# Kernel optimization log

Hardware: AMD Instinct MI355X
Metric: run time of the kernel (lower is better)

Reference implementation:

```python
import jax, jax.numpy as jnp
import numpy as np
import math

N_HEAD = 16
K_SPARSE = 64

def setup_inputs() -> dict:
    key = jax.random.key(0)
    ks = jax.random.split(key, 12)
    B, T, C = 1, 2048, 1024
    s = 0.02
    return {
        "x":   jax.random.normal(ks[0], (B, T, C), jnp.float32),
        "Wq":  jax.random.normal(ks[1], (C, C), jnp.float32) * s,
        "bq":  jax.random.normal(ks[2], (C,), jnp.float32) * s,
        "Wk":  jax.random.normal(ks[3], (C, C), jnp.float32) * s,
        "bk":  jax.random.normal(ks[4], (C,), jnp.float32) * s,
        "Wv":  jax.random.normal(ks[5], (C, C), jnp.float32) * s,
        "bv":  jax.random.normal(ks[6], (C,), jnp.float32) * s,
        "Wo":  jax.random.normal(ks[7], (C, C), jnp.float32) * s,
        "bo":  jax.random.normal(ks[8], (C,), jnp.float32) * s,
        "Wks": jax.random.normal(ks[9], (C,), jnp.float32) * s,
        "bks": jax.random.normal(ks[10], (), jnp.float32) * s,
    }

def reference(x, Wq, bq, Wk, bk, Wv, bv, Wo, bo, Wks, bks):
    B, T, C = x.shape
    nh = N_HEAD
    hs = C // nh
    k_val = min(K_SPARSE, T)

    # projections -> (B, nh, T, hs)   (torch Linear: x @ W.T + b)
    q = (x @ Wq.T + bq).reshape(B, T, nh, hs).transpose(0, 2, 1, 3)
    k = (x @ Wk.T + bk).reshape(B, T, nh, hs).transpose(0, 2, 1, 3)
    v = (x @ Wv.T + bv).reshape(B, T, nh, hs).transpose(0, 2, 1, 3)

    # key scorer: per-token scalar score (B, T)
    key_scores = x @ Wks + bks

    # causal masking of scores, then per-query top-k key selection
    pos = jnp.arange(T)
    causal = pos[None, :] <= pos[:, None]                      # (T, T), True where key<=query
    masked = jnp.where(causal[None], key_scores[:, None, :], -jnp.inf)  # (B, T, T)
    _, top_k_idx = jax.lax.top_k(masked, k_val)                # (B, T, k)
    top_k_idx = jnp.minimum(top_k_idx, pos[None, :, None])     # clamp to <= query pos

    # gather sparse keys/values: (B, nh, T, k, hs)
    bi = jnp.arange(B)[:, None, None, None]
    hi = jnp.arange(nh)[None, :, None, None]
    gi = top_k_idx[:, None, :, :]                              # (B, 1, T, k)
    sparse_k = k[bi, hi, gi]                                   # (B, nh, T, k, hs)
    sparse_v = v[bi, hi, gi]

    scale = 1.0 / math.sqrt(hs)
    logits = jnp.einsum('bhtd,bhtkd->bhtk', q, sparse_k) * scale
    probs = jax.nn.softmax(logits, axis=-1)
    out = jnp.einsum('bhtk,bhtkd->bhtd', probs, sparse_v)      # (B, nh, T, hs)
    out = out.transpose(0, 2, 1, 3).reshape(B, T, C)
    return out @ Wo.T + bo
```

## Files before the change

kernel.cpp:

```cpp
#include <hip/hip_runtime.h>
#include <hip/hip_bf16.h>
#include <cstdint>
#include <cstddef>

#define T_DIM 2048
#define C_DIM 1024
#define NH 16
#define HS 64
#define KSP 64

#define GBM 128
#define GBN 64
#define GBK 128
#define OBM 64
#define OBN 64

typedef short short8 __attribute__((ext_vector_type(8)));
typedef float f32x4 __attribute__((ext_vector_type(4)));
typedef _Float16 half2_t __attribute__((ext_vector_type(2)));

__device__ __forceinline__ float bfu2f(unsigned short u) {
  unsigned v = ((unsigned)u) << 16;
  return __builtin_bit_cast(float, v);
}
__device__ __forceinline__ unsigned short f2bfu(float f) {
  unsigned u = __builtin_bit_cast(unsigned, f);
  unsigned r = (u + 0x7fffu + ((u >> 16) & 1u)) >> 16;
  return (unsigned short)r;
}
__device__ __forceinline__ unsigned short f2h(float f) {
  _Float16 h = (_Float16)f;
  return __builtin_bit_cast(unsigned short, h);
}
__device__ __forceinline__ float bflo(unsigned u) {
  return __builtin_bit_cast(float, u << 16);
}
__device__ __forceinline__ float bfhi(unsigned u) {
  return __builtin_bit_cast(float, u & 0xffff0000u);
}

__device__ __forceinline__ float dot2h(unsigned kbits, unsigned qbits, float acc) {
#if __has_builtin(__builtin_amdgcn_fdot2)
  return __builtin_amdgcn_fdot2(__builtin_bit_cast(half2_t, kbits),
                                __builtin_bit_cast(half2_t, qbits), acc, false);
#else
  half2_t kk = __builtin_bit_cast(half2_t, kbits);
  half2_t qq = __builtin_bit_cast(half2_t, qbits);
  return acc + (float)kk.x * (float)qq.x + (float)kk.y * (float)qq.y;
#endif
}

#define GLOAD_LDS16(gp, lp)                                                  \
  __builtin_amdgcn_global_load_lds(                                          \
      (const __attribute__((address_space(1))) void*)(gp),                   \
      (__attribute__((address_space(3))) void*)(lp), 16, 0, 0)

#define NSCORE (T_DIM / 4)
#define NCONV ((T_DIM * C_DIM + 4 * C_DIM * C_DIM) / 4 / 256)
__global__ __launch_bounds__(256) void convert_scores_kernel(
    const float* __restrict__ x, const float* __restrict__ Wq,
    const float* __restrict__ Wk, const float* __restrict__ Wv,
    const float* __restrict__ Wo, const float* __restrict__ Wks,
    const float* __restrict__ bks,
    unsigned short* __restrict__ xb, unsigned short* __restrict__ Wqb,
    unsigned short* __restrict__ Wkb, unsigned short* __restrict__ Wvb,
    unsigned short* __restrict__ Wob, float* __restrict__ scores) {
  if (blockIdx.x < NSCORE) {
    const int t = blockIdx.x * 4 + (threadIdx.x >> 6);
    const int lane = threadIdx.x & 63;
    const float* xrow = x + (size_t)t * C_DIM;
    float acc = 0.f;
    #pragma unroll 4
    for (int i = lane; i < C_DIM; i += 64)
      acc += xrow[i] * Wks[i];
    #pragma unroll
    for (int o = 32; o; o >>= 1) acc += __shfl_xor(acc, o);
    if (lane == 0) scores[t] = acc + bks[0];
    return;
  }
  const int i = (blockIdx.x - NSCORE) * 256 + threadIdx.x;
  const int NX4 = T_DIM * C_DIM / 4;
  const int NW4 = C_DIM * C_DIM / 4;
  const float* src;
  unsigned short* dst;
  int j = i;
  if (j < NX4) { src = x; dst = xb; }
  else {
    j -= NX4;
    int w = j / NW4;
    j -= w * NW4;
    src = (w == 0) ? Wq : (w == 1) ? Wk : (w == 2) ? Wv : Wo;
    dst = (w == 0) ? Wqb : (w == 1) ? Wkb : (w == 2) ? Wvb : Wob;
  }
  float4 f = reinterpret_cast<const float4*>(src)[j];
  ushort4 o;
  o.x = f2bfu(f.x); o.y = f2bfu(f.y); o.z = f2bfu(f.z); o.w = f2bfu(f.w);
  reinterpret_cast<ushort4*>(dst)[j] = o;
}

__global__ __launch_bounds__(256) void rank_sort_kernel(
    const float* __restrict__ scores, int* __restrict__ sorted_idx) {
  __shared__ float ss[T_DIM];
  const int tid = threadIdx.x;
  for (int j = tid; j < T_DIM; j += 256) ss[j] = scores[j];
  __syncthreads();
  const int w = tid >> 6, lane = tid & 63;
  const int i = blockIdx.x * 4 + w;
  const float si = ss[i];
  int rank = 0;
  #pragma unroll
  for (int step = 0; step < T_DIM / 64; ++step) {
    const int j = step * 64 + lane;
    const float sj = ss[j];
    rank += (int)((sj > si) || (sj == si && j < i));
  }
  #pragma unroll
  for (int o = 32; o; o >>= 1) rank += __shfl_xor(rank, o);
  if (lane == 0) sorted_idx[rank] = i;
}

__global__ __launch_bounds__(256) void select_topk_kernel(
    const int* __restrict__ sorted_idx, int* __restrict__ topk) {
  __shared__ int ss[T_DIM];
  const int tid = threadIdx.x;
  for (int i = tid; i < T_DIM; i += 256) {
    int s = sorted_idx[i];
    ss[i] = (s < 0) ? 0 : (s > T_DIM - 1 ? T_DIM - 1 : s);
  }
  __syncthreads();
  const int t = blockIdx.x * 4 + (tid >> 6);
  const int lane = tid & 63;
  if (t <= 63) {
    topk[(size_t)t * KSP + lane] = (lane < t) ? lane : t;
  } else {
    const unsigned long long lt_mask = (1ull << lane) - 1ull;
    int count = 0;
    for (int chunk = 0; chunk < T_DIM / 64 && count < KSP; ++chunk) {
      int s = ss[chunk * 64 + lane];
      bool ok = (s <= t);
      unsigned long long m = __ballot(ok);
      int pos = count + __popcll(m & lt_mask);
      if (ok && pos < KSP) topk[(size_t)t * KSP + pos] = s;
      count += __popcll(m);
    }
  }
}

__device__ __forceinline__ void gemm_body_128x64(
    const unsigned short* __restrict__ A, const unsigned short* __restrict__ W,
    f32x4 acc[4][2], int bm, int bn, int tid) {
  __shared__ unsigned short As[GBM * GBK];
  __shared__ unsigned short Ws[GBN * GBK];
  const int w = tid >> 6, lane = tid & 63;
  const int quad = lane >> 4, r = lane & 15;
  const int wm = (w >> 1) * 64, wn = (w & 1) * 32;
  const int sub = lane >> 4;
  const int c = lane & 15;
  const unsigned short* Arow[8];
  const unsigned short* Wrow[4];
  #pragma unroll
  for (int i = 0; i < 8; ++i) {
    const int row = w * 32 + i * 4 + sub;
    Arow[i] = A + (size_t)(bm * GBM + row) * C_DIM + ((c ^ (row & 7)) * 8);
  }
  #pragma unroll
  for (int i = 0; i < 4; ++i) {
    const int row = w * 16 + i * 4 + sub;
    Wrow[i] = W + (size_t)(bn * GBN + row) * C_DIM + ((c ^ (row & 7)) * 8);
  }
  for (int kb = 0; kb < C_DIM; kb += GBK) {
    #pragma unroll
    for (int i = 0; i < 8; ++i)
      GLOAD_LDS16(Arow[i] + kb, &As[(w * 32 + i * 4) * GBK]);
    #pragma unroll
    for (int i = 0; i < 4; ++i)
      GLOAD_LDS16(Wrow[i] + kb, &Ws[(w * 16 + i * 4) * GBK]);
    __syncthreads();
    #pragma unroll
    for (int ks = 0; ks < 4; ++ks) {
      const int pc = ((ks * 4 + quad) ^ (r & 7)) * 8;
      short8 af[4], bfr[2];
      #pragma unroll
      for (int mi = 0; mi < 4; ++mi)
        af[mi] = *reinterpret_cast<const short8*>(&As[(wm + mi * 16 + r) * GBK + pc]);
      #pragma unroll
      for (int ni = 0; ni < 2; ++ni)
        bfr[ni] = *reinterpret_cast<const short8*>(&Ws[(wn + ni * 16 + r) * GBK + pc]);
      #pragma unroll
      for (int mi = 0; mi < 4; ++mi)
        #pragma unroll
        for (int ni = 0; ni < 2; ++ni)
          acc[mi][ni] = __builtin_amdgcn_mfma_f32_16x16x32_bf16(af[mi], bfr[ni], acc[mi][ni], 0, 0, 0);
    }
    __syncthreads();
  }
}

__global__ __launch_bounds__(256) void gemm_qkv_kernel(
    const unsigned short* __restrict__ A,
    const unsigned short* __restrict__ Wq, const unsigned short* __restrict__ Wk,
    const unsigned short* __restrict__ Wv,
    const float* __restrict__ bq, const float* __restrict__ bk,
    const float* __restrict__ bv,
    unsigned short* __restrict__ qo, unsigned short* __restrict__ ko,
    unsigned short* __restrict__ vo) {
  const int per = (T_DIM / GBM) * (C_DIM / GBN);
  const int which = blockIdx.x / per;
  const int rem = blockIdx.x % per;
  const int bm = rem / (C_DIM / GBN);
  const int bn = rem % (C_DIM / GBN);
  const unsigned short* W = (which == 0) ? Wq : (which == 1) ? Wk : Wv;
  const float* bias = (which == 0) ? bq : (which == 1) ? bk : bv;
  unsigned short* out = (which == 0) ? qo : (which == 1) ? ko : vo;
  const int tid = threadIdx.x;
  f32x4 acc[4][2] = {};
  gemm_body_128x64(A, W, acc, bm, bn, tid);
  const int w = tid >> 6, lane = tid & 63;
  const int quad = lane >> 4, r = lane & 15;
  const int wm = (w >> 1) * 64, wn = (w & 1) * 32;
  #pragma unroll
  for (int mi = 0; mi < 4; ++mi) {
    #pragma unroll
    for (int ni = 0; ni < 2; ++ni) {
      const int col = bn * GBN + wn + ni * 16 + r;
      const float bf = bias[col];
      #pragma unroll
      for (int i = 0; i < 4; ++i) {
        const int row = bm * GBM + wm + mi * 16 + quad * 4 + i;
        const float val = acc[mi][ni][i] + bf;
        out[(size_t)row * C_DIM + col] = (which == 2) ? f2bfu(val) : f2h(val);
      }
    }
  }
}

__device__ __forceinline__ void gemm_body_64x64(
    const unsigned short* __restrict__ A, const unsigned short* __restrict__ W,
    f32x4 acc[2][2], int bm, int bn, int tid) {
  __shared__ unsigned short As[OBM * GBK];
  __shared__ unsigned short Ws[OBN * GBK];
  const int w = tid >> 6, lane = tid & 63;
  const int quad = lane >> 4, r = lane & 15;
  const int wm = (w >> 1) * 32, wn = (w & 1) * 32;
  const int sub = lane >> 4;
  const int c = lane & 15;
  const unsigned short* Arow[4];
  const unsigned short* Wrow[4];
  #pragma unroll
  for (int i = 0; i < 4; ++i) {
    const int row = w * 16 + i * 4 + sub;
    Arow[i] = A + (size_t)(bm * OBM + row) * C_DIM + ((c ^ (row & 7)) * 8);
    Wrow[i] = W + (size_t)(bn * OBN + row) * C_DIM + ((c ^ (row & 7)) * 8);
  }
  for (int kb = 0; kb < C_DIM; kb += GBK) {
    #pragma unroll
    for (int i = 0; i < 4; ++i)
      GLOAD_LDS16(Arow[i] + kb, &As[(w * 16 + i * 4) * GBK]);
    #pragma unroll
    for (int i = 0; i < 4; ++i)
      GLOAD_LDS16(Wrow[i] + kb, &Ws[(w * 16 + i * 4) * GBK]);
    __syncthreads();
    #pragma unroll
    for (int ks = 0; ks < 4; ++ks) {
      const int pc = ((ks * 4 + quad) ^ (r & 7)) * 8;
      short8 af[2], bfr[2];
      #pragma unroll
      for (int mi = 0; mi < 2; ++mi)
        af[mi] = *reinterpret_cast<const short8*>(&As[(wm + mi * 16 + r) * GBK + pc]);
      #pragma unroll
      for (int ni = 0; ni < 2; ++ni)
        bfr[ni] = *reinterpret_cast<const short8*>(&Ws[(wn + ni * 16 + r) * GBK + pc]);
      #pragma unroll
      for (int mi = 0; mi < 2; ++mi)
        #pragma unroll
        for (int ni = 0; ni < 2; ++ni)
          acc[mi][ni] = __builtin_amdgcn_mfma_f32_16x16x32_bf16(af[mi], bfr[ni], acc[mi][ni], 0, 0, 0);
    }
    __syncthreads();
  }
}

__global__ __launch_bounds__(256) void gemm_o_f32_kernel(
    const unsigned short* __restrict__ A, const unsigned short* __restrict__ W,
    const float* __restrict__ bias, float* __restrict__ out) {
  const int tid = threadIdx.x;
  const int bm = blockIdx.x / (C_DIM / OBN);
  const int bn = blockIdx.x % (C_DIM / OBN);
  f32x4 acc[2][2] = {};
  gemm_body_64x64(A, W, acc, bm, bn, tid);
  const int w = tid >> 6, lane = tid & 63;
  const int quad = lane >> 4, r = lane & 15;
  const int wm = (w >> 1) * 32, wn = (w & 1) * 32;
  #pragma unroll
  for (int mi = 0; mi < 2; ++mi) {
    #pragma unroll
    for (int ni = 0; ni < 2; ++ni) {
      const int col = bn * OBN + wn + ni * 16 + r;
      const float bf = bias[col];
      #pragma unroll
      for (int i = 0; i < 4; ++i) {
        const int row = bm * OBM + wm + mi * 16 + quad * 4 + i;
        out[(size_t)row * C_DIM + col] = acc[mi][ni][i] + bf;
      }
    }
  }
}

__global__ __launch_bounds__(256) void attn_kernel(
    const unsigned short* __restrict__ q, const unsigned short* __restrict__ k,
    const unsigned short* __restrict__ v, const int* __restrict__ topk,
    unsigned short* __restrict__ attn_out) {
  __shared__ int off_s[4][KSP];
  const int t = blockIdx.x >> 2;
  const int hg = blockIdx.x & 3;
  const int tid = threadIdx.x;
  const int w = tid >> 6, lane = tid & 63;
  const int h = hg * 4 + w;
  const int c8 = lane & 7;
  const int ksub = lane >> 3;
  {
    int s = topk[(size_t)t * KSP + lane];
    s = (s < 0) ? 0 : (s > t ? t : s);
    off_s[w][lane] = s * C_DIM;
  }
  const int hbase = h * HS + 8 * c8;
  uint4 qraw = *reinterpret_cast<const uint4*>(q + (size_t)t * C_DIM + hbase);
  __builtin_amdgcn_wave_barrier();
  int offr[8];
  #pragma unroll
  for (int jj = 0; jj < 8; ++jj) offr[jj] = off_s[w][8 * jj + ksub];
  uint4 kraw[8], vraw[8];
  #pragma unroll
  for (int jj = 0; jj < 8; ++jj)
    kraw[jj] = *reinterpret_cast<const uint4*>(k + offr[jj] + hbase);
  #pragma unroll
  for (int jj = 0; jj < 8; ++jj)
    vraw[jj] = *reinterpret_cast<const uint4*>(v + offr[jj] + hbase);
  float l[8];
  #pragma unroll
  for (int jj = 0; jj < 8; ++jj) {
    const uint4 raw = kraw[jj];
    float pl = dot2h(raw.x, qraw.x, 0.f);
    pl = dot2h(raw.y, qraw.y, pl);
    pl = dot2h(raw.z, qraw.z, pl);
    pl = dot2h(raw.w, qraw.w, pl);
    pl *= 0.125f;
    pl += __shfl_xor(pl, 1);
    pl += __shfl_xor(pl, 2);
    pl += __shfl_xor(pl, 4);
    l[jj] = pl;
  }
  float m = l[0];
  #pragma unroll
  for (int jj = 1; jj < 8; ++jj) m = fmaxf(m, l[jj]);
  m = fmaxf(m, __shfl_xor(m, 8));
  m = fmaxf(m, __shfl_xor(m, 16));
  m = fmaxf(m, __shfl_xor(m, 32));
  float sum = 0.f;
  #pragma unroll
  for (int jj = 0; jj < 8; ++jj) {
    l[jj] = __expf(l[jj] - m);
    sum += l[jj];
  }
  sum += __shfl_xor(sum, 8);
  sum += __shfl_xor(sum, 16);
  sum += __shfl_xor(sum, 32);
  const float rs = 1.0f / sum;
  float a[8] = {0.f, 0.f, 0.f, 0.f, 0.f, 0.f, 0.f, 0.f};
  #pragma unroll
  for (int jj = 0; jj < 8; ++jj) {
    const uint4 raw = vraw[jj];
    const float p = l[jj] * rs;
    a[0] += p * bflo(raw.x); a[1] += p * bfhi(raw.x);
    a[2] += p * bflo(raw.y); a[3] += p * bfhi(raw.y);
    a[4] += p * bflo(raw.z); a[5] += p * bfhi(raw.z);
    a[6] += p * bflo(raw.w); a[7] += p * bfhi(raw.w);
  }
  #pragma unroll
  for (int o = 8; o <= 32; o <<= 1) {
    #pragma unroll
    for (int z = 0; z < 8; ++z) a[z] += __shfl_xor(a[z], o);
  }
  if (ksub == 0) {
    ushort4 o0, o1;
    o0.x = f2bfu(a[0]); o0.y = f2bfu(a[1]); o0.z = f2bfu(a[2]); o0.w = f2bfu(a[3]);
    o1.x = f2bfu(a[4]); o1.y = f2bfu(a[5]); o1.z = f2bfu(a[6]); o1.w = f2bfu(a[7]);
    ushort4* dst = reinterpret_cast<ushort4*>(attn_out + (size_t)t * C_DIM + hbase);
    dst[0] = o0;
    dst[1] = o1;
  }
}

extern "C" void kernel_launch(void* const* d_in, const int* in_sizes, int n_in,
                              void* d_out, int out_size, void* d_ws, size_t ws_size,
                              hipStream_t stream) {
  const float* x   = (const float*)d_in[0];
  const float* Wq  = (const float*)d_in[1];
  const float* bq  = (const float*)d_in[2];
  const float* Wk  = (const float*)d_in[3];
  const float* bk  = (const float*)d_in[4];
  const float* Wv  = (const float*)d_in[5];
  const float* bv  = (const float*)d_in[6];
  const float* Wo  = (const float*)d_in[7];
  const float* bo  = (const float*)d_in[8];
  const float* Wks = (const float*)d_in[9];
  const float* bks = (const float*)d_in[10];
  float* out = (float*)d_out;

  char* ws = (char*)d_ws;
  size_t off = 0;
  float* scores = (float*)(ws + off); off += 8192;
  int*   sorted = (int*)(ws + off);   off += 8192;
  int*   topk   = (int*)(ws + off);   off += (size_t)T_DIM * KSP * 4;
  unsigned short* xb  = (unsigned short*)(ws + off); off += (size_t)T_DIM * C_DIM * 2;
  unsigned short* Wqb = (unsigned short*)(ws + off); off += (size_t)C_DIM * C_DIM * 2;
  unsigned short* Wkb = (unsigned short*)(ws + off); off += (size_t)C_DIM * C_DIM * 2;
  unsigned short* Wvb = (unsigned short*)(ws + off); off += (size_t)C_DIM * C_DIM * 2;
  unsigned short* Wob = (unsigned short*)(ws + off); off += (size_t)C_DIM * C_DIM * 2;
  unsigned short* qb  = (unsigned short*)(ws + off); off += (size_t)T_DIM * C_DIM * 2;
  unsigned short* kb  = (unsigned short*)(ws + off); off += (size_t)T_DIM * C_DIM * 2;
  unsigned short* vb  = (unsigned short*)(ws + off); off += (size_t)T_DIM * C_DIM * 2;
  unsigned short* ab  = xb;

  convert_scores_kernel<<<NSCORE + NCONV, 256, 0, stream>>>(
      x, Wq, Wk, Wv, Wo, Wks, bks, xb, Wqb, Wkb, Wvb, Wob, scores);

  rank_sort_kernel<<<T_DIM / 4, 256, 0, stream>>>(scores, sorted);
  select_topk_kernel<<<T_DIM / 4, 256, 0, stream>>>(sorted, topk);

  gemm_qkv_kernel<<<3 * (T_DIM / GBM) * (C_DIM / GBN), 256, 0, stream>>>(
      xb, Wqb, Wkb, Wvb, bq, bk, bv, qb, kb, vb);

  attn_kernel<<<T_DIM * 4, 256, 0, stream>>>(qb, kb, vb, topk, ab);

  gemm_o_f32_kernel<<<(T_DIM / OBM) * (C_DIM / OBN), 256, 0, stream>>>(
      ab, Wob, bo, out);
}
```

Baseline: 155.6 us.

## Fuse rank sort into QKV GEMM launch and top-k selection into attention

The rank-sort pass now runs as extra blocks at the front of the QKV GEMM grid, sharing its LDS buffer. Top-k selection moves into the attention kernel, and the topk workspace array goes away. This removes two kernel launches and the global round-trip through topk. In exchange, every attention block (8192 of them) reloads the 2048-entry sorted array into LDS and runs the ballot scan per wave, which adds redundant work and LDS use to that kernel.

```diff
diff --git a/kernel.cpp b/kernel.cpp
--- a/kernel.cpp
+++ b/kernel.cpp
@@ -98,59 +98,10 @@
   reinterpret_cast<ushort4*>(dst)[j] = o;
 }
 
-__global__ __launch_bounds__(256) void rank_sort_kernel(
-    const float* __restrict__ scores, int* __restrict__ sorted_idx) {
-  __shared__ float ss[T_DIM];
-  const int tid = threadIdx.x;
-  for (int j = tid; j < T_DIM; j += 256) ss[j] = scores[j];
-  __syncthreads();
-  const int w = tid >> 6, lane = tid & 63;
-  const int i = blockIdx.x * 4 + w;
-  const float si = ss[i];
-  int rank = 0;
-  #pragma unroll
-  for (int step = 0; step < T_DIM / 64; ++step) {
-    const int j = step * 64 + lane;
-    const float sj = ss[j];
-    rank += (int)((sj > si) || (sj == si && j < i));
-  }
-  #pragma unroll
-  for (int o = 32; o; o >>= 1) rank += __shfl_xor(rank, o);
-  if (lane == 0) sorted_idx[rank] = i;
-}
-
-__global__ __launch_bounds__(256) void select_topk_kernel(
-    const int* __restrict__ sorted_idx, int* __restrict__ topk) {
-  __shared__ int ss[T_DIM];
-  const int tid = threadIdx.x;
-  for (int i = tid; i < T_DIM; i += 256) {
-    int s = sorted_idx[i];
-    ss[i] = (s < 0) ? 0 : (s > T_DIM - 1 ? T_DIM - 1 : s);
-  }
-  __syncthreads();
-  const int t = blockIdx.x * 4 + (tid >> 6);
-  const int lane = tid & 63;
-  if (t <= 63) {
-    topk[(size_t)t * KSP + lane] = (lane < t) ? lane : t;
-  } else {
-    const unsigned long long lt_mask = (1ull << lane) - 1ull;
-    int count = 0;
-    for (int chunk = 0; chunk < T_DIM / 64 && count < KSP; ++chunk) {
-      int s = ss[chunk * 64 + lane];
-      bool ok = (s <= t);
-      unsigned long long m = __ballot(ok);
-      int pos = count + __popcll(m & lt_mask);
-      if (ok && pos < KSP) topk[(size_t)t * KSP + pos] = s;
-      count += __popcll(m);
-    }
-  }
-}
-
 __device__ __forceinline__ void gemm_body_128x64(
     const unsigned short* __restrict__ A, const unsigned short* __restrict__ W,
-    f32x4 acc[4][2], int bm, int bn, int tid) {
-  __shared__ unsigned short As[GBM * GBK];
-  __shared__ unsigned short Ws[GBN * GBK];
+    f32x4 acc[4][2], int bm, int bn, int tid,
+    unsigned short* As, unsigned short* Ws) {
   const int w = tid >> 6, lane = tid & 63;
   const int quad = lane >> 4, r = lane & 15;
   const int wm = (w >> 1) * 64, wn = (w & 1) * 32;
@@ -196,25 +147,48 @@
   }
 }
 
-__global__ __launch_bounds__(256) void gemm_qkv_kernel(
+#define NRANK (T_DIM / 4)
+__global__ __launch_bounds__(256) void gemm_qkv_rank_kernel(
     const unsigned short* __restrict__ A,
     const unsigned short* __restrict__ Wq, const unsigned short* __restrict__ Wk,
     const unsigned short* __restrict__ Wv,
     const float* __restrict__ bq, const float* __restrict__ bk,
     const float* __restrict__ bv,
     unsigned short* __restrict__ qo, unsigned short* __restrict__ ko,
-    unsigned short* __restrict__ vo) {
+    unsigned short* __restrict__ vo,
+    const float* __restrict__ scores, int* __restrict__ sorted_idx) {
+  __shared__ unsigned short lds[(GBM + GBN) * GBK];
+  const int tid = threadIdx.x;
+  if (blockIdx.x < NRANK) {
+    float* ss = reinterpret_cast<float*>(lds);
+    for (int j = tid; j < T_DIM; j += 256) ss[j] = scores[j];
+    __syncthreads();
+    const int w = tid >> 6, lane = tid & 63;
+    const int i = blockIdx.x * 4 + w;
+    const float si = ss[i];
+    int rank = 0;
+    #pragma unroll
+    for (int step = 0; step < T_DIM / 64; ++step) {
+      const int j = step * 64 + lane;
+      const float sj = ss[j];
+      rank += (int)((sj > si) || (sj == si && j < i));
+    }
+    #pragma unroll
+    for (int o = 32; o; o >>= 1) rank += __shfl_xor(rank, o);
+    if (lane == 0) sorted_idx[rank] = i;
+    return;
+  }
+  const int bid = blockIdx.x - NRANK;
   const int per = (T_DIM / GBM) * (C_DIM / GBN);
-  const int which = blockIdx.x / per;
-  const int rem = blockIdx.x % per;
+  const int which = bid / per;
+  const int rem = bid % per;
   const int bm = rem / (C_DIM / GBN);
   const int bn = rem % (C_DIM / GBN);
   const unsigned short* W = (which == 0) ? Wq : (which == 1) ? Wk : Wv;
   const float* bias = (which == 0) ? bq : (which == 1) ? bk : bv;
   unsigned short* out = (which == 0) ? qo : (which == 1) ? ko : vo;
-  const int tid = threadIdx.x;
   f32x4 acc[4][2] = {};
-  gemm_body_128x64(A, W, acc, bm, bn, tid);
+  gemm_body_128x64(A, W, acc, bm, bn, tid, lds, lds + GBM * GBK);
   const int w = tid >> 6, lane = tid & 63;
   const int quad = lane >> 4, r = lane & 15;
   const int wm = (w >> 1) * 64, wn = (w & 1) * 32;
@@ -308,24 +282,39 @@
 
 __global__ __launch_bounds__(256) void attn_kernel(
     const unsigned short* __restrict__ q, const unsigned short* __restrict__ k,
-    const unsigned short* __restrict__ v, const int* __restrict__ topk,
+    const unsigned short* __restrict__ v, const int* __restrict__ sorted_idx,
     unsigned short* __restrict__ attn_out) {
+  __shared__ int ss[T_DIM];
   __shared__ int off_s[4][KSP];
   const int t = blockIdx.x >> 2;
   const int hg = blockIdx.x & 3;
   const int tid = threadIdx.x;
   const int w = tid >> 6, lane = tid & 63;
   const int h = hg * 4 + w;
+  for (int i = tid; i < T_DIM; i += 256) {
+    int s = sorted_idx[i];
+    ss[i] = (s < 0) ? 0 : (s > T_DIM - 1 ? T_DIM - 1 : s);
+  }
+  __syncthreads();
+  if (t <= 63) {
+    off_s[w][lane] = ((lane < t) ? lane : t) * C_DIM;
+  } else {
+    const unsigned long long lt_mask = (1ull << lane) - 1ull;
+    int count = 0;
+    for (int chunk = 0; chunk < T_DIM / 64 && count < KSP; ++chunk) {
+      int s = ss[chunk * 64 + lane];
+      bool ok = (s <= t);
+      unsigned long long mm = __ballot(ok);
+      int pos = count + __popcll(mm & lt_mask);
+      if (ok && pos < KSP) off_s[w][pos] = s * C_DIM;
+      count += __popcll(mm);
+    }
+  }
+  __builtin_amdgcn_wave_barrier();
   const int c8 = lane & 7;
   const int ksub = lane >> 3;
-  {
-    int s = topk[(size_t)t * KSP + lane];
-    s = (s < 0) ? 0 : (s > t ? t : s);
-    off_s[w][lane] = s * C_DIM;
-  }
   const int hbase = h * HS + 8 * c8;
   uint4 qraw = *reinterpret_cast<const uint4*>(q + (size_t)t * C_DIM + hbase);
-  __builtin_amdgcn_wave_barrier();
   int offr[8];
   #pragma unroll
   for (int jj = 0; jj < 8; ++jj) offr[jj] = off_s[w][8 * jj + ksub];
@@ -411,7 +400,6 @@
   size_t off = 0;
   float* scores = (float*)(ws + off); off += 8192;
   int*   sorted = (int*)(ws + off);   off += 8192;
-  int*   topk   = (int*)(ws + off);   off += (size_t)T_DIM * KSP * 4;
   unsigned short* xb  = (unsigned short*)(ws + off); off += (size_t)T_DIM * C_DIM * 2;
   unsigned short* Wqb = (unsigned short*)(ws + off); off += (size_t)C_DIM * C_DIM * 2;
   unsigned short* Wkb = (unsigned short*)(ws + off); off += (size_t)C_DIM * C_DIM * 2;
@@ -425,13 +413,11 @@
   convert_scores_kernel<<<NSCORE + NCONV, 256, 0, stream>>>(
       x, Wq, Wk, Wv, Wo, Wks, bks, xb, Wqb, Wkb, Wvb, Wob, scores);
 
-  rank_sort_kernel<<<T_DIM / 4, 256, 0, stream>>>(scores, sorted);
-  select_topk_kernel<<<T_DIM / 4, 256, 0, stream>>>(sorted, topk);
-
-  gemm_qkv_kernel<<<3 * (T_DIM / GBM) * (C_DIM / GBN), 256, 0, stream>>>(
-      xb, Wqb, Wkb, Wvb, bq, bk, bv, qb, kb, vb);
-
-  attn_kernel<<<T_DIM * 4, 256, 0, stream>>>(qb, kb, vb, topk, ab);
+  gemm_qkv_rank_kernel<<<NRANK + 3 * (T_DIM / GBM) * (C_DIM / GBN), 256, 0,
+                         stream>>>(
+      xb, Wqb, Wkb, Wvb, bq, bk, bv, qb, kb, vb, scores, sorted);
+
+  attn_kernel<<<T_DIM * 4, 256, 0, stream>>>(qb, kb, vb, sorted, ab);
 
   gemm_o_f32_kernel<<<(T_DIM / OBM) * (C_DIM / OBN), 256, 0, stream>>>(
       ab, Wob, bo, out);
```

Measured after the change: 155.1 us. Within noise of the previous version (-0.3%).
